# Kernel optimization log

Measured on AMD Instinct MI355X. Metric: run time of the kernel, lower is better.

The kernel has to match this reference:

```python
import jax, jax.numpy as jnp
import numpy as np

B, N = 1, 4096
D_IN, D_OUT, H = 256, 256, 8
HD = D_OUT // H
NEG = -9e15


def _xavier(key, shape):
    lim = np.sqrt(6.0 / (shape[0] + shape[1])).astype(np.float32)
    return jax.random.uniform(key, shape, jnp.float32, -lim, lim)


def setup_inputs() -> dict:
    key = jax.random.key(0)
    ks = jax.random.split(key, 8)
    x = jax.random.normal(ks[0], (B, N, D_IN), jnp.float32)
    adj = (jax.random.uniform(ks[1], (B, N, N)) < 0.05).astype(jnp.float32)
    idx = jnp.arange(N)
    adj = adj.at[:, idx, idx].set(1.0)
    Wq = _xavier(ks[2], (D_IN, D_OUT)); bq = jnp.zeros((D_OUT,), jnp.float32)
    Wk = _xavier(ks[3], (D_IN, D_OUT)); bk = jnp.zeros((D_OUT,), jnp.float32)
    Wv = _xavier(ks[4], (D_IN, D_OUT)); bv = jnp.zeros((D_OUT,), jnp.float32)
    Wo = _xavier(ks[5], (D_OUT, D_OUT)); bo = jnp.zeros((D_OUT,), jnp.float32)
    return dict(x=x, adj=adj, Wq=Wq, bq=bq, Wk=Wk, bk=bk, Wv=Wv, bv=bv, Wo=Wo, bo=bo)


def reference(x, adj, Wq, bq, Wk, bk, Wv, bv, Wo, bo):
    b, n, _ = x.shape
    def split_heads(t):  # [B,N,D_OUT] -> [B,H,N,HD]
        return t.reshape(b, n, H, HD).transpose(0, 2, 1, 3)
    q = split_heads(x @ Wq + bq)
    k = split_heads(x @ Wk + bk)
    v = split_heads(x @ Wv + bv)
    scores = jnp.einsum('bhqd,bhkd->bhqk', q, k) / np.float32(np.sqrt(HD))
    scores = jnp.where(adj[:, None, :, :] > 0, scores, jnp.float32(NEG))
    attn = jax.nn.softmax(scores, axis=-1)
    # dropout is identity in eval mode (training=False)
    out = jnp.einsum('bhqk,bhkd->bhqd', attn, v)
    out = out.transpose(0, 2, 1, 3).reshape(b, n, D_OUT)
    return out @ Wo + bo
```

## Files before the change

### kernel.cpp

```cpp
#include <hip/hip_runtime.h>
#include <hip/hip_bf16.h>
#include <stdint.h>

#define NTOK 4096
#define DIM  256
#define NH   8
#define HD   32
#define MAXNNZ 512

typedef __attribute__((ext_vector_type(8))) short short8;
typedef __attribute__((ext_vector_type(4))) float float4v;
typedef unsigned short u16;
typedef unsigned int u32;

__device__ __forceinline__ float bf2f(u16 u) {
    union { u32 u; float f; } c; c.u = ((u32)u) << 16; return c.f;
}
__device__ __forceinline__ u16 f2bf(float f) {
    union { float f; u32 u; } c; c.f = f;
    u32 u = c.u;
    u = u + 0x7FFFu + ((u >> 16) & 1u);
    return (u16)(u >> 16);
}
__device__ __forceinline__ float blo(u32 c) {
    union { u32 u; float f; } x; x.u = c << 16; return x.f;
}
__device__ __forceinline__ float bhi(u32 c) {
    union { u32 u; float f; } x; x.u = c & 0xFFFF0000u; return x.f;
}

__global__ void x_to_bf16(const float* __restrict__ x, u16* __restrict__ xb) {
    int i = (blockIdx.x * blockDim.x + threadIdx.x) * 4;
    float4 v = *(const float4*)(x + i);
    ushort4 o;
    o.x = f2bf(v.x); o.y = f2bf(v.y); o.z = f2bf(v.z); o.w = f2bf(v.w);
    *(ushort4*)(xb + i) = o;
}

__global__ void transpose_w(const float* __restrict__ Wq, const float* __restrict__ Wk,
                            const float* __restrict__ Wv, const float* __restrict__ Wo,
                            u16* __restrict__ WT) {
    const float* srcs[4] = {Wq, Wk, Wv, Wo};
    const float* W = srcs[blockIdx.y];
    int o = blockIdx.x, i = threadIdx.x;
    WT[blockIdx.y * 65536 + o * 256 + i] = f2bf(W[i * 256 + o]);
}

__global__ __launch_bounds__(256) void adj_to_list(const float* __restrict__ adj,
                                                   u16* __restrict__ NL,
                                                   u32* __restrict__ NC) {
    __shared__ u32 cnt;
    int row = blockIdx.x, t = threadIdx.x;
    if (t == 0) cnt = 0;
    __syncthreads();
    const float4* rp = (const float4*)(adj + (size_t)row * NTOK);
    u16* lbase = NL + (size_t)row * MAXNNZ;
#pragma unroll
    for (int i = 0; i < 4; ++i) {
        float4 v = rp[i * 256 + t];
        u32 m = 0;
        if (v.x != 0.f) m |= 1u;
        if (v.y != 0.f) m |= 2u;
        if (v.z != 0.f) m |= 4u;
        if (v.w != 0.f) m |= 8u;
        if (m) {
            int p = __popc(m);
            u32 base = atomicAdd(&cnt, (u32)p);
            int col0 = (i * 256 + t) * 4;
            while (m) {
                int j = __builtin_ctz(m);
                m &= m - 1;
                if (base < MAXNNZ) lbase[base] = (u16)(col0 + j);
                ++base;
            }
        }
    }
    __syncthreads();
    if (t == 0) NC[row] = (cnt < MAXNNZ) ? cnt : MAXNNZ;
}

__global__ __launch_bounds__(64) void qkv_gemm(
    const u16* __restrict__ xb,
    const u16* __restrict__ WT,
    const float* __restrict__ bq, const float* __restrict__ bk, const float* __restrict__ bv,
    u16* __restrict__ Q, u16* __restrict__ K, u16* __restrict__ V) {
    int lane = threadIdx.x, quad = lane >> 4, l16 = lane & 15;
    int mtile = blockIdx.x, ntile = blockIdx.y, mat = blockIdx.z;
    const float* bias = (mat == 0) ? bq : (mat == 1) ? bk : bv;
    const u16* arow = xb + (size_t)(mtile * 16 + l16) * DIM + quad * 8;
    const u16* brow = WT + (size_t)mat * 65536 + (size_t)(ntile * 16 + l16) * DIM + quad * 8;
    float4v acc = {0.f, 0.f, 0.f, 0.f};
#pragma unroll
    for (int k0 = 0; k0 < DIM; k0 += 32) {
        short8 af = *(const short8*)(arow + k0);
        short8 bf = *(const short8*)(brow + k0);
        acc = __builtin_amdgcn_mfma_f32_16x16x32_bf16(af, bf, acc, 0, 0, 0);
    }
    int n = ntile * 16 + l16;
    float bb = bias[n];
    const float sc = (mat == 0) ? 0.25503635559913516f : 1.0f;
    u16* dst = (mat == 0) ? Q : (mat == 1) ? K : V;
#pragma unroll
    for (int r = 0; r < 4; ++r) {
        int m = mtile * 16 + quad * 4 + r;
        dst[(size_t)m * DIM + n] = f2bf((acc[r] + bb) * sc);
    }
}

__global__ __launch_bounds__(256, 4) void sparse_attn(
    const u16* __restrict__ Q, const u16* __restrict__ K, const u16* __restrict__ V,
    const u16* __restrict__ NL, const u32* __restrict__ NC,
    u16* __restrict__ AO) {
    int row = blockIdx.x * 4 + (threadIdx.x >> 6);
    int lane = threadIdx.x & 63;
    int p = lane >> 5;
    int t = lane & 31;

    uint4 qq = *(const uint4*)(Q + (size_t)row * DIM + t * 8);
    float q0 = blo(qq.x), q1 = bhi(qq.x), q2 = blo(qq.y), q3 = bhi(qq.y);
    float q4 = blo(qq.z), q5 = bhi(qq.z), q6 = blo(qq.w), q7 = bhi(qq.w);

    float O[8];
#pragma unroll
    for (int i = 0; i < 8; ++i) O[i] = 0.f;
    float lsum = 0.f;

    int nnz = (int)NC[row];
    const u16* lst = NL + (size_t)row * MAXNNZ;
    const u16* Kt = K + t * 8;
    const u16* Vt = V + t * 8;

#define PAIR_BODY(kk, vv, e_valid)                                               \
    {                                                                            \
        float a = 0.f, b = 0.f;                                                  \
        a = fmaf(blo(kk.x), q0, a); b = fmaf(bhi(kk.x), q1, b);                  \
        a = fmaf(blo(kk.y), q2, a); b = fmaf(bhi(kk.y), q3, b);                  \
        a = fmaf(blo(kk.z), q4, a); b = fmaf(bhi(kk.z), q5, b);                  \
        a = fmaf(blo(kk.w), q6, a); b = fmaf(bhi(kk.w), q7, b);                  \
        float s = a + b;                                                         \
        s += __shfl_xor(s, 1, 64);                                               \
        s += __shfl_xor(s, 2, 64);      \
        float e = __builtin_amdgcn_exp2f(s);                                     \
        e = (e_valid) ? e : 0.f;                                                 \
        lsum += e;                                                               \
        O[0] = fmaf(e, blo(vv.x), O[0]); O[1] = fmaf(e, bhi(vv.x), O[1]);        \
        O[2] = fmaf(e, blo(vv.y), O[2]); O[3] = fmaf(e, bhi(vv.y), O[3]);        \
        O[4] = fmaf(e, blo(vv.z), O[4]); O[5] = fmaf(e, bhi(vv.z), O[5]);        \
        O[6] = fmaf(e, blo(vv.w), O[6]); O[7] = fmaf(e, bhi(vv.w), O[7]);        \
    }

    u32 wA = *(const u32*)(lst);
    u32 wB = (nnz > 2) ? *(const u32*)(lst + 2) : wA;
    for (int i2 = 0; i2 < nnz; i2 += 4) {
        bool vA = (i2 + p) < nnz;
        bool vB = (i2 + 2 + p) < nnz;
        int lo = (int)(wA & 0xFFFFu);
        int iA = p ? (int)(wA >> 16) : lo;
        int iB = p ? (int)(wB >> 16) : (int)(wB & 0xFFFFu);
        if (!vA) iA = lo;
        if (!vB) iB = lo;

        int in0 = i2 + 4, in2 = i2 + 6;
        u32 wAn = *(const u32*)(lst + ((in0 < nnz) ? in0 : 0));
        u32 wBn = *(const u32*)(lst + ((in2 < nnz) ? in2 : 0));

        uint4 kA = *(const uint4*)(Kt + (size_t)iA * DIM);
        uint4 vAv = *(const uint4*)(Vt + (size_t)iA * DIM);
        uint4 kB = *(const uint4*)(Kt + (size_t)iB * DIM);
        uint4 vBv = *(const uint4*)(Vt + (size_t)iB * DIM);

        PAIR_BODY(kA, vAv, vA)
        PAIR_BODY(kB, vBv, vB)

        wA = wAn; wB = wBn;
    }
#undef PAIR_BODY

#pragma unroll
    for (int i = 0; i < 8; ++i) O[i] += __shfl_xor(O[i], 32, 64);
    lsum += __shfl_xor(lsum, 32, 64);

    if (p == 0) {
        float inv = 1.0f / lsum;
        u32 w0 = (u32)f2bf(O[0] * inv) | ((u32)f2bf(O[1] * inv) << 16);
        u32 w1 = (u32)f2bf(O[2] * inv) | ((u32)f2bf(O[3] * inv) << 16);
        u32 w2 = (u32)f2bf(O[4] * inv) | ((u32)f2bf(O[5] * inv) << 16);
        u32 w3 = (u32)f2bf(O[6] * inv) | ((u32)f2bf(O[7] * inv) << 16);
        *(uint4*)(AO + (size_t)row * DIM + t * 8) = make_uint4(w0, w1, w2, w3);
    }
}

__global__ __launch_bounds__(64) void out_gemm(
    const u16* __restrict__ AO, const u16* __restrict__ WTo, const float* __restrict__ bo,
    float* __restrict__ out) {
    int lane = threadIdx.x, quad = lane >> 4, l16 = lane & 15;
    int mtile = blockIdx.x, ntile = blockIdx.y;
    const u16* arow = AO + (size_t)(mtile * 16 + l16) * DIM + quad * 8;
    const u16* brow = WTo + (size_t)(ntile * 16 + l16) * DIM + quad * 8;
    float4v acc = {0.f, 0.f, 0.f, 0.f};
#pragma unroll
    for (int k0 = 0; k0 < DIM; k0 += 32) {
        short8 af = *(const short8*)(arow + k0);
        short8 bf = *(const short8*)(brow + k0);
        acc = __builtin_amdgcn_mfma_f32_16x16x32_bf16(af, bf, acc, 0, 0, 0);
    }
    int n = ntile * 16 + l16;
    float bb = bo[n];
#pragma unroll
    for (int r = 0; r < 4; ++r)
        out[(size_t)(mtile * 16 + quad * 4 + r) * DIM + n] = acc[r] + bb;
}

extern "C" void kernel_launch(void* const* d_in, const int* in_sizes, int n_in,
                              void* d_out, int out_size, void* d_ws, size_t ws_size,
                              hipStream_t stream) {
    const float* x   = (const float*)d_in[0];
    const float* adj = (const float*)d_in[1];
    const float* Wq  = (const float*)d_in[2];
    const float* bq  = (const float*)d_in[3];
    const float* Wk  = (const float*)d_in[4];
    const float* bk  = (const float*)d_in[5];
    const float* Wv  = (const float*)d_in[6];
    const float* bv  = (const float*)d_in[7];
    const float* Wo  = (const float*)d_in[8];
    const float* bo  = (const float*)d_in[9];

    char* ws = (char*)d_ws;
    const size_t MB = 1u << 20;
    u16* Q   = (u16*)(ws);
    u16* K   = (u16*)(ws + 2 * MB);
    u16* V   = (u16*)(ws + 4 * MB);
    u16* AO  = (u16*)(ws + 6 * MB);
    u16* WT  = (u16*)(ws + 8 * MB);
    u16* XB  = (u16*)(ws + 8 * MB + 512 * 1024);
    u16* NL  = (u16*)(ws + 11 * MB);
    u32* NC  = (u32*)(ws + 15 * MB);

    x_to_bf16<<<dim3(1024), 256, 0, stream>>>(x, XB);
    transpose_w<<<dim3(256, 4), 256, 0, stream>>>(Wq, Wk, Wv, Wo, WT);
    adj_to_list<<<dim3(4096), 256, 0, stream>>>(adj, NL, NC);
    qkv_gemm<<<dim3(256, 16, 3), 64, 0, stream>>>(XB, WT, bq, bk, bv, Q, K, V);
    sparse_attn<<<dim3(1024), 256, 0, stream>>>(Q, K, V, NL, NC, AO);
    out_gemm<<<dim3(256, 16), 64, 0, stream>>>(AO, WT + 3 * 65536, bo, (float*)d_out);
}
```

Baseline: 199.9 us.

## Split each attention row's neighbor list across two wavefronts and reduce via LDS

Each query row is now handled by two wavefronts that each process half of the neighbor list, doubling the grid to 2048 blocks of two rows each. Partial outputs and softmax sums from the second half are combined through shared memory after a block barrier. The launch bound is raised to 8 blocks per CU. This shortens the per-wave serial gather loop and exposes more memory-level parallelism, at the cost of an LDS reduction and a barrier.

```diff
diff --git a/kernel.cpp b/kernel.cpp
--- a/kernel.cpp
+++ b/kernel.cpp
@@ -107,14 +107,18 @@
     }
 }
 
-__global__ __launch_bounds__(256, 4) void sparse_attn(
+__global__ __launch_bounds__(256, 8) void sparse_attn(
     const u16* __restrict__ Q, const u16* __restrict__ K, const u16* __restrict__ V,
     const u16* __restrict__ NL, const u32* __restrict__ NC,
     u16* __restrict__ AO) {
-    int row = blockIdx.x * 4 + (threadIdx.x >> 6);
-    int lane = threadIdx.x & 63;
+    __shared__ float part[2][32][9];
+    int tid  = threadIdx.x;
+    int rb   = tid >> 7;
+    int half = (tid >> 6) & 1;
+    int lane = tid & 63;
     int p = lane >> 5;
     int t = lane & 31;
+    int row = blockIdx.x * 2 + rb;
 
     uint4 qq = *(const uint4*)(Q + (size_t)row * DIM + t * 8);
     float q0 = blo(qq.x), q1 = bhi(qq.x), q2 = blo(qq.y), q3 = bhi(qq.y);
@@ -127,6 +131,9 @@
 
     int nnz = (int)NC[row];
     const u16* lst = NL + (size_t)row * MAXNNZ;
+    int nh    = ((nnz + 4) >> 3) << 2;
+    int begin = half ? nh : 0;
+    int end   = half ? nnz : nh;
     const u16* Kt = K + t * 8;
     const u16* Vt = V + t * 8;
 
@@ -149,30 +156,32 @@
         O[6] = fmaf(e, blo(vv.w), O[6]); O[7] = fmaf(e, bhi(vv.w), O[7]);        \
     }
 
-    u32 wA = *(const u32*)(lst);
-    u32 wB = (nnz > 2) ? *(const u32*)(lst + 2) : wA;
-    for (int i2 = 0; i2 < nnz; i2 += 4) {
-        bool vA = (i2 + p) < nnz;
-        bool vB = (i2 + 2 + p) < nnz;
-        int lo = (int)(wA & 0xFFFFu);
-        int iA = p ? (int)(wA >> 16) : lo;
-        int iB = p ? (int)(wB >> 16) : (int)(wB & 0xFFFFu);
-        if (!vA) iA = lo;
-        if (!vB) iB = lo;
-
-        int in0 = i2 + 4, in2 = i2 + 6;
-        u32 wAn = *(const u32*)(lst + ((in0 < nnz) ? in0 : 0));
-        u32 wBn = *(const u32*)(lst + ((in2 < nnz) ? in2 : 0));
-
-        uint4 kA = *(const uint4*)(Kt + (size_t)iA * DIM);
-        uint4 vAv = *(const uint4*)(Vt + (size_t)iA * DIM);
-        uint4 kB = *(const uint4*)(Kt + (size_t)iB * DIM);
-        uint4 vBv = *(const uint4*)(Vt + (size_t)iB * DIM);
-
-        PAIR_BODY(kA, vAv, vA)
-        PAIR_BODY(kB, vBv, vB)
-
-        wA = wAn; wB = wBn;
+    if (begin < end) {
+        u32 wA = *(const u32*)(lst + begin);
+        u32 wB = (begin + 2 < end) ? *(const u32*)(lst + begin + 2) : wA;
+        for (int i2 = begin; i2 < end; i2 += 4) {
+            bool vA = (i2 + p) < end;
+            bool vB = (i2 + 2 + p) < end;
+            int lo = (int)(wA & 0xFFFFu);
+            int iA = p ? (int)(wA >> 16) : lo;
+            int iB = p ? (int)(wB >> 16) : (int)(wB & 0xFFFFu);
+            if (!vA) iA = lo;
+            if (!vB) iB = lo;
+
+            int in0 = i2 + 4, in2 = i2 + 6;
+            u32 wAn = *(const u32*)(lst + ((in0 < end) ? in0 : begin));
+            u32 wBn = *(const u32*)(lst + ((in2 < end) ? in2 : begin));
+
+            uint4 kA  = *(const uint4*)(Kt + (size_t)iA * DIM);
+            uint4 vAv = *(const uint4*)(Vt + (size_t)iA * DIM);
+            uint4 kB  = *(const uint4*)(Kt + (size_t)iB * DIM);
+            uint4 vBv = *(const uint4*)(Vt + (size_t)iB * DIM);
+
+            PAIR_BODY(kA, vAv, vA)
+            PAIR_BODY(kB, vBv, vB)
+
+            wA = wAn; wB = wBn;
+        }
     }
 #undef PAIR_BODY
 
@@ -180,7 +189,16 @@
     for (int i = 0; i < 8; ++i) O[i] += __shfl_xor(O[i], 32, 64);
     lsum += __shfl_xor(lsum, 32, 64);
 
-    if (p == 0) {
+    if (half == 1 && p == 0) {
+#pragma unroll
+        for (int i = 0; i < 8; ++i) part[rb][t][i] = O[i];
+        part[rb][t][8] = lsum;
+    }
+    __syncthreads();
+    if (half == 0 && p == 0) {
+#pragma unroll
+        for (int i = 0; i < 8; ++i) O[i] += part[rb][t][i];
+        lsum += part[rb][t][8];
         float inv = 1.0f / lsum;
         u32 w0 = (u32)f2bf(O[0] * inv) | ((u32)f2bf(O[1] * inv) << 16);
         u32 w1 = (u32)f2bf(O[2] * inv) | ((u32)f2bf(O[3] * inv) << 16);
@@ -240,6 +258,6 @@
     transpose_w<<<dim3(256, 4), 256, 0, stream>>>(Wq, Wk, Wv, Wo, WT);
     adj_to_list<<<dim3(4096), 256, 0, stream>>>(adj, NL, NC);
     qkv_gemm<<<dim3(256, 16, 3), 64, 0, stream>>>(XB, WT, bq, bk, bv, Q, K, V);
-    sparse_attn<<<dim3(1024), 256, 0, stream>>>(Q, K, V, NL, NC, AO);
+    sparse_attn<<<dim3(2048), 256, 0, stream>>>(Q, K, V, NL, NC, AO);
     out_gemm<<<dim3(256, 16), 64, 0, stream>>>(AO, WT + 3 * 65536, bo, (float*)d_out);
 }
```

Measured after the change: 197.0 us. Within noise of the previous version (-1.5%).
